# Performance work log

Hardware: AMD Instinct MI355X
Metric: run time of the kernel (lower is better)

The kernel has to match this reference:

```python
import jax, jax.numpy as jnp
import numpy as np

B = 16384
TEXT_DIM = 768
AUDIO_DIM = 1024
E = 1024
H = 8
DH = E // H


def setup_inputs() -> dict:
    key = jax.random.key(0)
    ks = jax.random.split(key, 20)
    s_in = lambda d: 1.0 / np.sqrt(d)
    inp = {
        'text_emb': jax.random.normal(ks[0], (B, TEXT_DIM), jnp.float32),
        'audio_emb': jax.random.normal(ks[1], (B, AUDIO_DIM), jnp.float32),
        # modality projections
        'Wt': jax.random.uniform(ks[2], (E, TEXT_DIM), jnp.float32, -s_in(TEXT_DIM), s_in(TEXT_DIM)),
        'bt': jnp.zeros((E,), jnp.float32),
        'Wa': jax.random.uniform(ks[3], (E, AUDIO_DIM), jnp.float32, -s_in(AUDIO_DIM), s_in(AUDIO_DIM)),
        'ba': jnp.zeros((E,), jnp.float32),
        # shared MultiheadAttention (packed in_proj split into q/k/v)
        'Wq': jax.random.uniform(ks[4], (E, E), jnp.float32, -s_in(E), s_in(E)),
        'bq': jnp.zeros((E,), jnp.float32),
        'Wk': jax.random.uniform(ks[5], (E, E), jnp.float32, -s_in(E), s_in(E)),
        'bk': jnp.zeros((E,), jnp.float32),
        'Wv': jax.random.uniform(ks[6], (E, E), jnp.float32, -s_in(E), s_in(E)),
        'bv': jnp.zeros((E,), jnp.float32),
        'Wo': jax.random.uniform(ks[7], (E, E), jnp.float32, -s_in(E), s_in(E)),
        'bo': jnp.zeros((E,), jnp.float32),
        # sigmoid gates
        'Wgt': jax.random.uniform(ks[8], (E, 2 * E), jnp.float32, -s_in(2 * E), s_in(2 * E)),
        'bgt': jnp.zeros((E,), jnp.float32),
        'Wga': jax.random.uniform(ks[9], (E, 2 * E), jnp.float32, -s_in(2 * E), s_in(2 * E)),
        'bga': jnp.zeros((E,), jnp.float32),
    }
    return inp


def _mha(q_in, kv_in, Wq, bq, Wk, bk, Wv, bv, Wo, bo):
    # seq_len == 1 for both query and key/value: tensors are (B, E)
    q = (q_in @ Wq.T + bq).reshape(B, H, DH)
    k = (kv_in @ Wk.T + bk).reshape(B, H, DH)
    v = (kv_in @ Wv.T + bv).reshape(B, H, DH)
    scores = jnp.einsum('bhd,bhd->bh', q, k) / np.sqrt(DH)  # (B, H), single kv slot
    w = jax.nn.softmax(scores[..., None], axis=-1)          # softmax over kv axis (size 1) -> ones
    ctx = (w * v).reshape(B, E)
    return ctx @ Wo.T + bo


def reference(text_emb, audio_emb, Wt, bt, Wa, ba, Wq, bq, Wk, bk, Wv, bv, Wo, bo, Wgt, bgt, Wga, bga):
    t = text_emb @ Wt.T + bt      # (B, E)
    a = audio_emb @ Wa.T + ba     # (B, E)
    t_ctx = _mha(t, a, Wq, bq, Wk, bk, Wv, bv, Wo, bo)
    a_ctx = _mha(a, t, Wq, bq, Wk, bk, Wv, bv, Wo, bo)
    g_t = jax.nn.sigmoid(jnp.concatenate([t, t_ctx], axis=-1) @ Wgt.T + bgt)
    refined_t = g_t * t + (1.0 - g_t) * t_ctx
    g_a = jax.nn.sigmoid(jnp.concatenate([a, a_ctx], axis=-1) @ Wga.T + bga)
    refined_a = g_a * a + (1.0 - g_a) * a_ctx
    return refined_t, refined_a
```

## Files before the change

kernel.cpp:

```cpp
#include <hip/hip_runtime.h>
#include <hip/hip_bf16.h>


typedef __attribute__((ext_vector_type(8))) short short8;
typedef __attribute__((ext_vector_type(4))) float floatx4;

#define WAITV(N) asm volatile("s_waitcnt vmcnt(" #N ")" ::: "memory")
__device__ __forceinline__ void blockbar() {
  asm volatile("" ::: "memory");
  __builtin_amdgcn_s_barrier();
  asm volatile("" ::: "memory");
}

__device__ __forceinline__ float bf2f(__hip_bfloat16 x) { return __bfloat162float(x); }

__device__ __forceinline__ void gl_lds16(const void* g, void* l) {
  __builtin_amdgcn_global_load_lds(
      (const __attribute__((address_space(1))) unsigned int*)g,
      (__attribute__((address_space(3))) unsigned int*)l,
      16, 0, 0);
}

__device__ __forceinline__ void swizzle_mn(int& m_idx, int& n_idx) {
  const int lid = blockIdx.y * 8 + blockIdx.x;
  m_idx = (lid >> 6) * 8 + (lid & 7);
  n_idx = (lid >> 3) & 7;
}

__global__ __launch_bounds__(256)
void cvt_kernel(const float* __restrict__ src, int sld,
                __hip_bfloat16* __restrict__ dst, int dld, int cols4) {
  const int r = blockIdx.y;
  const int c4 = blockIdx.x * 256 + threadIdx.x;
  if (c4 >= cols4) return;
  const float4 v = *(const float4*)(src + (size_t)r * sld + c4 * 4);
  union { __hip_bfloat16 h[4]; uint2 u; } o;
  o.h[0] = __float2bfloat16(v.x);
  o.h[1] = __float2bfloat16(v.y);
  o.h[2] = __float2bfloat16(v.z);
  o.h[3] = __float2bfloat16(v.w);
  *(uint2*)(dst + (size_t)r * dld + c4 * 4) = o.u;
}

__global__ __launch_bounds__(256)
void cvt_t_kernel(const float* __restrict__ src, __hip_bfloat16* __restrict__ dst,
                  int R, int C) {
  __shared__ float tile[32][33];
  const int tx = threadIdx.x, ty = threadIdx.y;
  const int bx = blockIdx.x * 32, by = blockIdx.y * 32;
#pragma unroll
  for (int i = 0; i < 32; i += 8)
    tile[ty + i][tx] = src[(size_t)(by + ty + i) * C + bx + tx];
  __syncthreads();
#pragma unroll
  for (int i = 0; i < 32; i += 8)
    dst[(size_t)(bx + ty + i) * R + by + tx] = __float2bfloat16(tile[tx][ty + i]);
}

__global__ __launch_bounds__(256)
void mv_kernel(const float* __restrict__ W, int ld, int coff,
               const float* __restrict__ x, const float* __restrict__ b,
               float* __restrict__ y) {
  const int lane = threadIdx.x & 63;
  const int row = blockIdx.x * 4 + (threadIdx.x >> 6);
  float acc = 0.f;
  for (int k = lane; k < 1024; k += 64)
    acc += W[(size_t)row * ld + coff + k] * x[k];
#pragma unroll
  for (int off = 32; off > 0; off >>= 1) acc += __shfl_down(acc, off);
  if (lane == 0) y[row] = acc + b[row];
}

__global__ __launch_bounds__(256)
void gemm_bt_kernel(const __hip_bfloat16* __restrict__ A,
                    const __hip_bfloat16* __restrict__ W,
                    const float* __restrict__ bias,
                    __hip_bfloat16* __restrict__ C,
                    int K, int ldc, int coff) {
  constexpr int BK = 32;
  __shared__ __align__(16) __hip_bfloat16 lA[2 * 128 * BK];
  __shared__ __align__(16) __hip_bfloat16 lB[2 * 128 * BK];

  const int tid  = threadIdx.x;
  const int lane = tid & 63;
  const int wave = tid >> 6;
  const int wm = wave & 1;
  const int wn = wave >> 1;
  int m_idx, n_idx;
  swizzle_mn(m_idx, n_idx);
  const int m0 = m_idx * 128;
  const int n0 = n_idx * 128;

  floatx4 acc[4][4];
#pragma unroll
  for (int i = 0; i < 4; ++i)
#pragma unroll
    for (int j = 0; j < 4; ++j) {
      floatx4 z = {0.f, 0.f, 0.f, 0.f};
      acc[i][j] = z;
    }

  const int srow  = tid >> 2;
  const int sc_sw = ((tid & 3) ^ (srow & 3)) * 8;
  const int fr = lane & 15;
  const int fq = (((lane >> 4) ^ (fr & 3))) * 8;

  const __hip_bfloat16* pA = A + (size_t)(m0 + srow) * K + sc_sw;
  const __hip_bfloat16* pW = W + (size_t)(n0 + srow) * K + sc_sw;
  const size_t SR = (size_t)64 * K;

  auto stageAB = [&](int buf) {
    gl_lds16(pA,      (char*)lA + buf * 8192 + tid * 16);
    gl_lds16(pA + SR, (char*)lA + buf * 8192 + 4096 + tid * 16);
    gl_lds16(pW,      (char*)lB + buf * 8192 + tid * 16);
    gl_lds16(pW + SR, (char*)lB + buf * 8192 + 4096 + tid * 16);
    pA += BK; pW += BK;
  };

  auto compute = [&](int cur) {
    const short* sA = (const short*)lA + cur * 4096;
    const short* sB = (const short*)lB + cur * 4096;
    short8 af[4], bfr[4];
#pragma unroll
    for (int i = 0; i < 4; ++i)
      af[i] = *(const short8*)(sA + (wm * 64 + i * 16 + fr) * BK + fq);
#pragma unroll
    for (int j = 0; j < 4; ++j)
      bfr[j] = *(const short8*)(sB + (wn * 64 + j * 16 + fr) * BK + fq);
#pragma unroll
    for (int i = 0; i < 4; ++i)
#pragma unroll
      for (int j = 0; j < 4; ++j)
        acc[i][j] = __builtin_amdgcn_mfma_f32_16x16x32_bf16(af[i], bfr[j], acc[i][j], 0, 0, 0);
  };

  const int NT = K / BK;
  stageAB(0);
  for (int t = 0; t < NT - 1; ++t) {
    const int cur = t & 1;
    stageAB(cur ^ 1);
    WAITV(4);
    blockbar();
    compute(cur);
    blockbar();
  }
  WAITV(0);
  blockbar();
  compute((NT - 1) & 1);

  const int col = lane & 15;
  const int rq  = (lane >> 4) * 4;
#pragma unroll
  for (int j = 0; j < 4; ++j) {
    const int n = n0 + wn * 64 + j * 16 + col;
    const float bv = bias ? bias[n] : 0.f;
#pragma unroll
    for (int i = 0; i < 4; ++i)
#pragma unroll
      for (int r = 0; r < 4; ++r) {
        const int m = m0 + wm * 64 + i * 16 + rq + r;
        C[(size_t)m * ldc + coff + n] = __float2bfloat16(acc[i][j][r] + bv);
      }
  }
}

__global__ __launch_bounds__(256)
void fused_gate_kernel(const __hip_bfloat16* __restrict__ Xs,
                       const __hip_bfloat16* __restrict__ Xo,
                       const __hip_bfloat16* __restrict__ Wg1,
                       const __hip_bfloat16* __restrict__ Wg2vo,
                       const __hip_bfloat16* __restrict__ Wvo,
                       const float* __restrict__ bg,
                       const float* __restrict__ bvo,
                       float* __restrict__ out) {
  constexpr int BK = 32;
  __shared__ __align__(16) __hip_bfloat16 lA[2 * 128 * BK];
  __shared__ __align__(16) __hip_bfloat16 lB[2 * 128 * BK];
  __shared__ __align__(16) __hip_bfloat16 lC[2 * 128 * BK];

  const int tid  = threadIdx.x;
  const int lane = tid & 63;
  const int wave = tid >> 6;
  const int wm = wave & 1;
  const int wn = wave >> 1;
  int m_idx, n_idx;
  swizzle_mn(m_idx, n_idx);
  const int m0 = m_idx * 128;
  const int n0 = n_idx * 128;

  floatx4 accL[4][4], accC[4][4];
#pragma unroll
  for (int i = 0; i < 4; ++i)
#pragma unroll
    for (int j = 0; j < 4; ++j) {
      floatx4 z = {0.f, 0.f, 0.f, 0.f};
      accL[i][j] = z;
      accC[i][j] = z;
    }

  const int srow  = tid >> 2;
  const int sc_sw = ((tid & 3) ^ (srow & 3)) * 8;
  const int fr = lane & 15;
  const int fq = (((lane >> 4) ^ (fr & 3))) * 8;

  const __hip_bfloat16* pAs = Xs    + (size_t)(m0 + srow) * 1024 + sc_sw;
  const __hip_bfloat16* pB1 = Wg1   + (size_t)(n0 + srow) * 1024 + sc_sw;
  const __hip_bfloat16* pAo = Xo    + (size_t)(m0 + srow) * 1024 + sc_sw;
  const __hip_bfloat16* pB2 = Wg2vo + (size_t)(n0 + srow) * 1024 + sc_sw;
  const __hip_bfloat16* pBv = Wvo   + (size_t)(n0 + srow) * 1024 + sc_sw;
  const size_t SR = (size_t)64 * 1024;

  auto stage1 = [&](int buf) {
    gl_lds16(pAs,      (char*)lA + buf * 8192 + tid * 16);
    gl_lds16(pAs + SR, (char*)lA + buf * 8192 + 4096 + tid * 16);
    gl_lds16(pB1,      (char*)lB + buf * 8192 + tid * 16);
    gl_lds16(pB1 + SR, (char*)lB + buf * 8192 + 4096 + tid * 16);
    pAs += BK; pB1 += BK;
  };
  auto stage2 = [&](int buf) {
    gl_lds16(pAo,      (char*)lA + buf * 8192 + tid * 16);
    gl_lds16(pAo + SR, (char*)lA + buf * 8192 + 4096 + tid * 16);
    gl_lds16(pB2,      (char*)lB + buf * 8192 + tid * 16);
    gl_lds16(pB2 + SR, (char*)lB + buf * 8192 + 4096 + tid * 16);
    gl_lds16(pBv,      (char*)lC + buf * 8192 + tid * 16);
    gl_lds16(pBv + SR, (char*)lC + buf * 8192 + 4096 + tid * 16);
    pAo += BK; pB2 += BK; pBv += BK;
  };

  auto comp1 = [&](int cur) {
    const short* sA = (const short*)lA + cur * 4096;
    const short* sB = (const short*)lB + cur * 4096;
    short8 af[4], bfr[4];
#pragma unroll
    for (int i = 0; i < 4; ++i)
      af[i] = *(const short8*)(sA + (wm * 64 + i * 16 + fr) * BK + fq);
#pragma unroll
    for (int j = 0; j < 4; ++j)
      bfr[j] = *(const short8*)(sB + (wn * 64 + j * 16 + fr) * BK + fq);
#pragma unroll
    for (int i = 0; i < 4; ++i)
#pragma unroll
      for (int j = 0; j < 4; ++j)
        accL[i][j] = __builtin_amdgcn_mfma_f32_16x16x32_bf16(af[i], bfr[j], accL[i][j], 0, 0, 0);
  };
  auto comp2 = [&](int cur) {
    const short* sA = (const short*)lA + cur * 4096;
    const short* sB = (const short*)lB + cur * 4096;
    const short* sC = (const short*)lC + cur * 4096;
    short8 af[4], bfr[4], cfr[4];
#pragma unroll
    for (int i = 0; i < 4; ++i)
      af[i] = *(const short8*)(sA + (wm * 64 + i * 16 + fr) * BK + fq);
#pragma unroll
    for (int j = 0; j < 4; ++j) {
      bfr[j] = *(const short8*)(sB + (wn * 64 + j * 16 + fr) * BK + fq);
      cfr[j] = *(const short8*)(sC + (wn * 64 + j * 16 + fr) * BK + fq);
    }
#pragma unroll
    for (int i = 0; i < 4; ++i)
#pragma unroll
      for (int j = 0; j < 4; ++j) {
        accL[i][j] = __builtin_amdgcn_mfma_f32_16x16x32_bf16(af[i], bfr[j], accL[i][j], 0, 0, 0);
        accC[i][j] = __builtin_amdgcn_mfma_f32_16x16x32_bf16(af[i], cfr[j], accC[i][j], 0, 0, 0);
      }
  };

  stage1(0);
  for (int t = 0; t < 31; ++t) {
    stage1((t & 1) ^ 1);
    WAITV(4);
    blockbar();
    comp1(t & 1);
    blockbar();
  }
  stage2(0);
  WAITV(6);
  blockbar();
  comp1(1);
  blockbar();
  for (int t = 0; t < 31; ++t) {
    stage2((t & 1) ^ 1);
    WAITV(6);
    blockbar();
    comp2(t & 1);
    blockbar();
  }
  WAITV(0);
  blockbar();
  comp2(1);

  const int col = lane & 15;
  const int rq  = (lane >> 4) * 4;
#pragma unroll
  for (int j = 0; j < 4; ++j) {
    const int n = n0 + wn * 64 + j * 16 + col;
    const float bgv = bg[n];
    const float bcv = bvo[n];
#pragma unroll
    for (int i = 0; i < 4; ++i)
#pragma unroll
      for (int r = 0; r < 4; ++r) {
        const int m = m0 + wm * 64 + i * 16 + rq + r;
        const size_t idx = (size_t)m * 1024 + n;
        const float lg = accL[i][j][r] + bgv;
        const float cv = accC[i][j][r] + bcv;
        const float xv = bf2f(Xs[idx]);
        const float g = 1.f / (1.f + __expf(-lg));
        out[idx] = g * xv + (1.f - g) * cv;
      }
  }
}

extern "C" void kernel_launch(void* const* d_in, const int* in_sizes, int n_in,
                              void* d_out, int out_size, void* d_ws, size_t ws_size,
                              hipStream_t stream) {
  (void)in_sizes; (void)n_in; (void)out_size; (void)ws_size;

  const float* text  = (const float*)d_in[0];
  const float* audio = (const float*)d_in[1];
  const float* Wt  = (const float*)d_in[2];
  const float* bt  = (const float*)d_in[3];
  const float* Wa  = (const float*)d_in[4];
  const float* ba  = (const float*)d_in[5];
  const float* Wv  = (const float*)d_in[10];
  const float* bv  = (const float*)d_in[11];
  const float* Wo  = (const float*)d_in[12];
  const float* bo  = (const float*)d_in[13];
  const float* Wgt = (const float*)d_in[14];
  const float* bgt = (const float*)d_in[15];
  const float* Wga = (const float*)d_in[16];
  const float* bga = (const float*)d_in[17];

  const size_t BE = 16384ull * 1024;
  const size_t M1 = 1024ull * 1024;
  float* out = (float*)d_out;

  __hip_bfloat16* p = (__hip_bfloat16*)d_ws;
  __hip_bfloat16* X      = p; p += 2 * BE;
  __hip_bfloat16* Wt_b   = p; p += 768ull * 1024;
  __hip_bfloat16* Wa_b   = p; p += M1;
  __hip_bfloat16* Wo_b   = p; p += M1;
  __hip_bfloat16* Wvo_b  = p; p += M1;
  __hip_bfloat16* Wg1t_b = p; p += M1;
  __hip_bfloat16* Wg1a_b = p; p += M1;
  __hip_bfloat16* G2vo   = p; p += 2 * M1;
  float* bvo  = (float*)p;
  float* bgtp = bvo + 1024;
  float* bgap = bvo + 2048;

  __hip_bfloat16* scr     = (__hip_bfloat16*)d_out;
  __hip_bfloat16* text_b  = scr;
  __hip_bfloat16* audio_b = scr + 16384ull * 768;
  __hip_bfloat16* WvT_b   = audio_b + BE;
  __hip_bfloat16* WvoT_b  = WvT_b + M1;
  __hip_bfloat16* G2      = WvoT_b + M1;

  dim3 blk(256, 1, 1);

  cvt_kernel<<<dim3(1, 16384), blk, 0, stream>>>(text, 768, text_b, 768, 192);
  cvt_kernel<<<dim3(1, 16384), blk, 0, stream>>>(audio, 1024, audio_b, 1024, 256);
  cvt_kernel<<<dim3(1, 768), blk, 0, stream>>>(Wt, 1024, Wt_b, 1024, 256);
  cvt_kernel<<<dim3(1, 1024), blk, 0, stream>>>(Wa, 1024, Wa_b, 1024, 256);
  cvt_kernel<<<dim3(1, 1024), blk, 0, stream>>>(Wo, 1024, Wo_b, 1024, 256);
  cvt_t_kernel<<<dim3(32, 32), dim3(32, 8), 0, stream>>>(Wv, WvT_b, 1024, 1024);
  cvt_kernel<<<dim3(1, 1024), blk, 0, stream>>>(Wgt, 2048, Wg1t_b, 1024, 256);
  cvt_kernel<<<dim3(1, 1024), blk, 0, stream>>>(Wgt + 1024, 2048, G2, 1024, 256);
  cvt_kernel<<<dim3(1, 1024), blk, 0, stream>>>(Wga, 2048, Wg1a_b, 1024, 256);
  cvt_kernel<<<dim3(1, 1024), blk, 0, stream>>>(Wga + 1024, 2048, G2 + M1, 1024, 256);

  mv_kernel<<<dim3(256), blk, 0, stream>>>(Wo, 1024, 0, bv, bo, bvo);
  mv_kernel<<<dim3(256), blk, 0, stream>>>(Wgt, 2048, 1024, bvo, bgt, bgtp);
  mv_kernel<<<dim3(256), blk, 0, stream>>>(Wga, 2048, 1024, bvo, bga, bgap);

  gemm_bt_kernel<<<dim3(8, 8), blk, 0, stream>>>(Wo_b, WvT_b, nullptr, Wvo_b, 1024, 1024, 0);
  gemm_bt_kernel<<<dim3(8, 8), blk, 0, stream>>>(WvT_b, Wo_b, nullptr, WvoT_b, 1024, 1024, 0);
  gemm_bt_kernel<<<dim3(8, 16), blk, 0, stream>>>(G2, WvoT_b, nullptr, G2vo, 1024, 1024, 0);

  dim3 g1(8, 128);
  gemm_bt_kernel<<<g1, blk, 0, stream>>>(text_b, Wt_b, bt, X, 768, 1024, 0);
  gemm_bt_kernel<<<g1, blk, 0, stream>>>(audio_b, Wa_b, ba, X + BE, 1024, 1024, 0);

  fused_gate_kernel<<<g1, blk, 0, stream>>>(X, X + BE, Wg1t_b, G2vo, Wvo_b, bgtp, bvo, out);
  fused_gate_kernel<<<g1, blk, 0, stream>>>(X + BE, X, Wg1a_b, G2vo + M1, Wvo_b, bgap, bvo, out + BE);
}
```

Measured before the change: 727.6 us.

## Batch conversion, projection and gate launches; triple-buffer GEMM staging

Folds the nine fp32-to-bf16 conversions into one multi-job kernel and pairs the two gate-bias matvecs into one launch. The text and audio projection GEMMs now run as a single grid, and both gate kernels run as one grid. The redundant WvT·Wo GEMM is replaced by a bf16 transpose of Wvo. The GEMM moves from double to triple LDS buffering, which drops the trailing barrier per K step. The aim is fewer launches, a less serialized tail, and less synchronization, at the cost of more LDS per block and per-block job selection.

```diff
diff --git a/kernel.cpp b/kernel.cpp
--- a/kernel.cpp
+++ b/kernel.cpp
@@ -27,19 +27,26 @@
   n_idx = (lid >> 3) & 7;
 }
 
-__global__ __launch_bounds__(256)
-void cvt_kernel(const float* __restrict__ src, int sld,
-                __hip_bfloat16* __restrict__ dst, int dld, int cols4) {
-  const int r = blockIdx.y;
-  const int c4 = blockIdx.x * 256 + threadIdx.x;
-  if (c4 >= cols4) return;
-  const float4 v = *(const float4*)(src + (size_t)r * sld + c4 * 4);
+struct CvtJob { const float* src; __hip_bfloat16* dst; int sld, dld, cols4, rowbase; };
+struct CvtJobs { CvtJob j[9]; };
+
+__global__ __launch_bounds__(256)
+void cvt9_kernel(CvtJobs a) {
+  const int r = blockIdx.x;
+  int ji = 0;
+#pragma unroll
+  for (int i = 1; i < 9; ++i) ji += (r >= a.j[i].rowbase) ? 1 : 0;
+  const CvtJob J = a.j[ji];
+  const int rr = r - J.rowbase;
+  const int c4 = threadIdx.x;
+  if (c4 >= J.cols4) return;
+  const float4 v = *(const float4*)(J.src + (size_t)rr * J.sld + c4 * 4);
   union { __hip_bfloat16 h[4]; uint2 u; } o;
   o.h[0] = __float2bfloat16(v.x);
   o.h[1] = __float2bfloat16(v.y);
   o.h[2] = __float2bfloat16(v.z);
   o.h[3] = __float2bfloat16(v.w);
-  *(uint2*)(dst + (size_t)r * dld + c4 * 4) = o.u;
+  *(uint2*)(J.dst + (size_t)rr * J.dld + c4 * 4) = o.u;
 }
 
 __global__ __launch_bounds__(256)
@@ -55,6 +62,21 @@
 #pragma unroll
   for (int i = 0; i < 32; i += 8)
     dst[(size_t)(bx + ty + i) * R + by + tx] = __float2bfloat16(tile[tx][ty + i]);
+}
+
+__global__ __launch_bounds__(256)
+void tr_bf16_kernel(const __hip_bfloat16* __restrict__ src,
+                    __hip_bfloat16* __restrict__ dst) {
+  __shared__ __hip_bfloat16 tile[32][33];
+  const int tx = threadIdx.x, ty = threadIdx.y;
+  const int bx = blockIdx.x * 32, by = blockIdx.y * 32;
+#pragma unroll
+  for (int i = 0; i < 32; i += 8)
+    tile[ty + i][tx] = src[(size_t)(by + ty + i) * 1024 + bx + tx];
+  __syncthreads();
+#pragma unroll
+  for (int i = 0; i < 32; i += 8)
+    dst[(size_t)(bx + ty + i) * 1024 + by + tx] = tile[tx][ty + i];
 }
 
 __global__ __launch_bounds__(256)
@@ -72,14 +94,33 @@
 }
 
 __global__ __launch_bounds__(256)
-void gemm_bt_kernel(const __hip_bfloat16* __restrict__ A,
-                    const __hip_bfloat16* __restrict__ W,
-                    const float* __restrict__ bias,
-                    __hip_bfloat16* __restrict__ C,
-                    int K, int ldc, int coff) {
+void mv2_kernel(const float* __restrict__ W0, const float* __restrict__ W1,
+                const float* __restrict__ x,
+                const float* __restrict__ b0, const float* __restrict__ b1,
+                float* __restrict__ y0, float* __restrict__ y1) {
+  const float* W = blockIdx.y ? W1 : W0;
+  const float* b = blockIdx.y ? b1 : b0;
+  float* y = blockIdx.y ? y1 : y0;
+  const int lane = threadIdx.x & 63;
+  const int row = blockIdx.x * 4 + (threadIdx.x >> 6);
+  float acc = 0.f;
+  for (int k = lane; k < 1024; k += 64)
+    acc += W[(size_t)row * 2048 + 1024 + k] * x[k];
+#pragma unroll
+  for (int off = 32; off > 0; off >>= 1) acc += __shfl_down(acc, off);
+  if (lane == 0) y[row] = acc + b[row];
+}
+
+struct GemmJob {
+  const __hip_bfloat16* A; const __hip_bfloat16* W;
+  const float* bias; __hip_bfloat16* C; int K; int ldc; int coff;
+};
+
+__global__ __launch_bounds__(256)
+void gemm_bt2_kernel(GemmJob j0, GemmJob j1, int mSplit) {
   constexpr int BK = 32;
-  __shared__ __align__(16) __hip_bfloat16 lA[2 * 128 * BK];
-  __shared__ __align__(16) __hip_bfloat16 lB[2 * 128 * BK];
+  __shared__ __align__(16) __hip_bfloat16 lA[3 * 128 * BK];
+  __shared__ __align__(16) __hip_bfloat16 lB[3 * 128 * BK];
 
   const int tid  = threadIdx.x;
   const int lane = tid & 63;
@@ -88,8 +129,11 @@
   const int wn = wave >> 1;
   int m_idx, n_idx;
   swizzle_mn(m_idx, n_idx);
-  const int m0 = m_idx * 128;
+  const bool sec = m_idx >= mSplit;
+  const GemmJob J = sec ? j1 : j0;
+  const int m0 = (sec ? m_idx - mSplit : m_idx) * 128;
   const int n0 = n_idx * 128;
+  const int K = J.K;
 
   floatx4 acc[4][4];
 #pragma unroll
@@ -105,21 +149,23 @@
   const int fr = lane & 15;
   const int fq = (((lane >> 4) ^ (fr & 3))) * 8;
 
-  const __hip_bfloat16* pA = A + (size_t)(m0 + srow) * K + sc_sw;
-  const __hip_bfloat16* pW = W + (size_t)(n0 + srow) * K + sc_sw;
+  const __hip_bfloat16* pA = J.A + (size_t)(m0 + srow) * K + sc_sw;
+  const __hip_bfloat16* pW = J.W + (size_t)(n0 + srow) * K + sc_sw;
   const size_t SR = (size_t)64 * K;
 
-  auto stageAB = [&](int buf) {
-    gl_lds16(pA,      (char*)lA + buf * 8192 + tid * 16);
-    gl_lds16(pA + SR, (char*)lA + buf * 8192 + 4096 + tid * 16);
-    gl_lds16(pW,      (char*)lB + buf * 8192 + tid * 16);
-    gl_lds16(pW + SR, (char*)lB + buf * 8192 + 4096 + tid * 16);
+  int sOff = 0;
+  auto stageAB = [&]() {
+    gl_lds16(pA,      (char*)lA + sOff + tid * 16);
+    gl_lds16(pA + SR, (char*)lA + sOff + 4096 + tid * 16);
+    gl_lds16(pW,      (char*)lB + sOff + tid * 16);
+    gl_lds16(pW + SR, (char*)lB + sOff + 4096 + tid * 16);
     pA += BK; pW += BK;
-  };
-
-  auto compute = [&](int cur) {
-    const short* sA = (const short*)lA + cur * 4096;
-    const short* sB = (const short*)lB + cur * 4096;
+    sOff = (sOff == 16384) ? 0 : sOff + 8192;
+  };
+
+  auto compute = [&](int cOff) {
+    const short* sA = (const short*)((const char*)lA + cOff);
+    const short* sB = (const short*)((const char*)lB + cOff);
     short8 af[4], bfr[4];
 #pragma unroll
     for (int i = 0; i < 4; ++i)
@@ -135,42 +181,44 @@
   };
 
   const int NT = K / BK;
-  stageAB(0);
+  int cOff = 0;
+  stageAB();
   for (int t = 0; t < NT - 1; ++t) {
-    const int cur = t & 1;
-    stageAB(cur ^ 1);
+    stageAB();
     WAITV(4);
     blockbar();
-    compute(cur);
-    blockbar();
+    compute(cOff);
+    cOff = (cOff == 16384) ? 0 : cOff + 8192;
   }
   WAITV(0);
   blockbar();
-  compute((NT - 1) & 1);
+  compute(cOff);
 
   const int col = lane & 15;
   const int rq  = (lane >> 4) * 4;
 #pragma unroll
   for (int j = 0; j < 4; ++j) {
     const int n = n0 + wn * 64 + j * 16 + col;
-    const float bv = bias ? bias[n] : 0.f;
+    const float bv = J.bias ? J.bias[n] : 0.f;
 #pragma unroll
     for (int i = 0; i < 4; ++i)
 #pragma unroll
       for (int r = 0; r < 4; ++r) {
         const int m = m0 + wm * 64 + i * 16 + rq + r;
-        C[(size_t)m * ldc + coff + n] = __float2bfloat16(acc[i][j][r] + bv);
+        J.C[(size_t)m * J.ldc + J.coff + n] = __float2bfloat16(acc[i][j][r] + bv);
       }
   }
 }
 
 __global__ __launch_bounds__(256)
-void fused_gate_kernel(const __hip_bfloat16* __restrict__ Xs,
-                       const __hip_bfloat16* __restrict__ Xo,
-                       const __hip_bfloat16* __restrict__ Wg1,
-                       const __hip_bfloat16* __restrict__ Wg2vo,
+void fused_gate_kernel(const __hip_bfloat16* __restrict__ Xt,
+                       const __hip_bfloat16* __restrict__ Xa,
+                       const __hip_bfloat16* __restrict__ Wg1t,
+                       const __hip_bfloat16* __restrict__ Wg1a,
+                       const __hip_bfloat16* __restrict__ G2vo,
                        const __hip_bfloat16* __restrict__ Wvo,
-                       const float* __restrict__ bg,
+                       const float* __restrict__ bgt,
+                       const float* __restrict__ bga,
                        const float* __restrict__ bvo,
                        float* __restrict__ out) {
   constexpr int BK = 32;
@@ -185,8 +233,17 @@
   const int wn = wave >> 1;
   int m_idx, n_idx;
   swizzle_mn(m_idx, n_idx);
-  const int m0 = m_idx * 128;
+  const bool aud = m_idx >= 128;
+  const int m0 = (m_idx & 127) * 128;
   const int n0 = n_idx * 128;
+
+  const size_t M1 = 1024ull * 1024;
+  const __hip_bfloat16* Xs  = aud ? Xa : Xt;
+  const __hip_bfloat16* Xo  = aud ? Xt : Xa;
+  const __hip_bfloat16* Wg1 = aud ? Wg1a : Wg1t;
+  const __hip_bfloat16* Wg2vo = G2vo + (aud ? M1 : 0);
+  const float* bg = aud ? bga : bgt;
+  float* po = out + (aud ? (size_t)16384 * 1024 : 0);
 
   floatx4 accL[4][4], accC[4][4];
 #pragma unroll
@@ -306,7 +363,7 @@
         const float cv = accC[i][j][r] + bcv;
         const float xv = bf2f(Xs[idx]);
         const float g = 1.f / (1.f + __expf(-lg));
-        out[idx] = g * xv + (1.f - g) * cv;
+        po[idx] = g * xv + (1.f - g) * cv;
       }
   }
 }
@@ -357,29 +414,32 @@
 
   dim3 blk(256, 1, 1);
 
-  cvt_kernel<<<dim3(1, 16384), blk, 0, stream>>>(text, 768, text_b, 768, 192);
-  cvt_kernel<<<dim3(1, 16384), blk, 0, stream>>>(audio, 1024, audio_b, 1024, 256);
-  cvt_kernel<<<dim3(1, 768), blk, 0, stream>>>(Wt, 1024, Wt_b, 1024, 256);
-  cvt_kernel<<<dim3(1, 1024), blk, 0, stream>>>(Wa, 1024, Wa_b, 1024, 256);
-  cvt_kernel<<<dim3(1, 1024), blk, 0, stream>>>(Wo, 1024, Wo_b, 1024, 256);
+  CvtJobs cj;
+  cj.j[0] = { text,       text_b,  768,  768,  192, 0 };
+  cj.j[1] = { audio,      audio_b, 1024, 1024, 256, 16384 };
+  cj.j[2] = { Wt,         Wt_b,    1024, 1024, 256, 32768 };
+  cj.j[3] = { Wa,         Wa_b,    1024, 1024, 256, 33536 };
+  cj.j[4] = { Wo,         Wo_b,    1024, 1024, 256, 34560 };
+  cj.j[5] = { Wgt,        Wg1t_b,  2048, 1024, 256, 35584 };
+  cj.j[6] = { Wgt + 1024, G2,      2048, 1024, 256, 36608 };
+  cj.j[7] = { Wga,        Wg1a_b,  2048, 1024, 256, 37632 };
+  cj.j[8] = { Wga + 1024, G2 + M1, 2048, 1024, 256, 38656 };
+  cvt9_kernel<<<dim3(39680), blk, 0, stream>>>(cj);
   cvt_t_kernel<<<dim3(32, 32), dim3(32, 8), 0, stream>>>(Wv, WvT_b, 1024, 1024);
-  cvt_kernel<<<dim3(1, 1024), blk, 0, stream>>>(Wgt, 2048, Wg1t_b, 1024, 256);
-  cvt_kernel<<<dim3(1, 1024), blk, 0, stream>>>(Wgt + 1024, 2048, G2, 1024, 256);
-  cvt_kernel<<<dim3(1, 1024), blk, 0, stream>>>(Wga, 2048, Wg1a_b, 1024, 256);
-  cvt_kernel<<<dim3(1, 1024), blk, 0, stream>>>(Wga + 1024, 2048, G2 + M1, 1024, 256);
 
   mv_kernel<<<dim3(256), blk, 0, stream>>>(Wo, 1024, 0, bv, bo, bvo);
-  mv_kernel<<<dim3(256), blk, 0, stream>>>(Wgt, 2048, 1024, bvo, bgt, bgtp);
-  mv_kernel<<<dim3(256), blk, 0, stream>>>(Wga, 2048, 1024, bvo, bga, bgap);
-
-  gemm_bt_kernel<<<dim3(8, 8), blk, 0, stream>>>(Wo_b, WvT_b, nullptr, Wvo_b, 1024, 1024, 0);
-  gemm_bt_kernel<<<dim3(8, 8), blk, 0, stream>>>(WvT_b, Wo_b, nullptr, WvoT_b, 1024, 1024, 0);
-  gemm_bt_kernel<<<dim3(8, 16), blk, 0, stream>>>(G2, WvoT_b, nullptr, G2vo, 1024, 1024, 0);
-
-  dim3 g1(8, 128);
-  gemm_bt_kernel<<<g1, blk, 0, stream>>>(text_b, Wt_b, bt, X, 768, 1024, 0);
-  gemm_bt_kernel<<<g1, blk, 0, stream>>>(audio_b, Wa_b, ba, X + BE, 1024, 1024, 0);
-
-  fused_gate_kernel<<<g1, blk, 0, stream>>>(X, X + BE, Wg1t_b, G2vo, Wvo_b, bgtp, bvo, out);
-  fused_gate_kernel<<<g1, blk, 0, stream>>>(X + BE, X, Wg1a_b, G2vo + M1, Wvo_b, bgap, bvo, out + BE);
-}
+  mv2_kernel<<<dim3(256, 2), blk, 0, stream>>>(Wgt, Wga, bvo, bgt, bga, bgtp, bgap);
+
+  GemmJob f1 = { Wo_b, WvT_b, nullptr, Wvo_b, 1024, 1024, 0 };
+  gemm_bt2_kernel<<<dim3(8, 8), blk, 0, stream>>>(f1, f1, 999);
+  tr_bf16_kernel<<<dim3(32, 32), dim3(32, 8), 0, stream>>>(Wvo_b, WvoT_b);
+  GemmJob f3 = { G2, WvoT_b, nullptr, G2vo, 1024, 1024, 0 };
+  gemm_bt2_kernel<<<dim3(8, 16), blk, 0, stream>>>(f3, f3, 999);
+
+  GemmJob pt = { text_b,  Wt_b, bt, X,      768,  1024, 0 };
+  GemmJob pa = { audio_b, Wa_b, ba, X + BE, 1024, 1024, 0 };
+  gemm_bt2_kernel<<<dim3(8, 256), blk, 0, stream>>>(pt, pa, 128);
+
+  fused_gate_kernel<<<dim3(8, 256), blk, 0, stream>>>(
+      X, X + BE, Wg1t_b, Wg1a_b, G2vo, Wvo_b, bgtp, bgap, bvo, out);
+}
```

After: 639.9 us. 12.1% less time.
